# Performance work log

Measured on AMD Instinct MI355X. Metric: run time of the kernel, lower is better.

## Reference

```python
import jax, jax.numpy as jnp
import numpy as np

N_HARM_XYZ = 6
N_HARM_DIR = 4
HIDDEN_XYZ = 256
HIDDEN_DIR = 128
EMB_XYZ = N_HARM_XYZ * 2 * 3 + 3  # 39
EMB_DIR = N_HARM_DIR * 2 * 3 + 3  # 27


def harmonic_embedding(x, n_harmonics):
    # x: [..., 3] -> [..., n_harmonics*2*3 + 3]
    freqs = 2.0 ** jnp.arange(n_harmonics, dtype=x.dtype)  # logspace, omega0=1
    emb = (x[..., None] * freqs).reshape(*x.shape[:-1], -1)  # [..., 3*n_harm]
    return jnp.concatenate([jnp.sin(emb), jnp.cos(emb), x], axis=-1)


def setup_inputs() -> dict:
    key = jax.random.key(0)
    ks = jax.random.split(key, 32)
    R, P = 2048, 64
    inp = {
        'sample_points': jax.random.normal(ks[0], (R, P, 3), dtype=jnp.float32),
        'directions': jax.random.normal(ks[1], (R, 3), dtype=jnp.float32),
    }
    # trunk layer dims (skip concat before layer 5; last layer outputs hidden+1)
    dims_in = [EMB_XYZ, HIDDEN_XYZ, HIDDEN_XYZ, HIDDEN_XYZ, HIDDEN_XYZ,
               HIDDEN_XYZ + EMB_XYZ, HIDDEN_XYZ, HIDDEN_XYZ]
    dims_out = [HIDDEN_XYZ] * 7 + [HIDDEN_XYZ + 1]
    for i, (di, do) in enumerate(zip(dims_in, dims_out)):
        s = 1.0 / np.sqrt(di)
        inp[f'W{i}'] = jax.random.uniform(ks[2 + 2 * i], (di, do), jnp.float32, -s, s)
        inp[f'b{i}'] = jax.random.uniform(ks[3 + 2 * i], (do,), jnp.float32, -s, s)
    s = 1.0 / np.sqrt(HIDDEN_XYZ + EMB_DIR)
    inp['Wc'] = jax.random.uniform(ks[20], (HIDDEN_XYZ + EMB_DIR, HIDDEN_DIR), jnp.float32, -s, s)
    inp['bc'] = jax.random.uniform(ks[21], (HIDDEN_DIR,), jnp.float32, -s, s)
    s = 1.0 / np.sqrt(HIDDEN_DIR)
    inp['Wo'] = jax.random.uniform(ks[22], (HIDDEN_DIR, 3), jnp.float32, -s, s)
    inp['bo'] = jax.random.uniform(ks[23], (3,), jnp.float32, -s, s)
    return inp


def nerf_forward(sample_points, directions,
                 W0, b0, W1, b1, W2, b2, W3, b3, W4, b4, W5, b5, W6, b6, W7, b7,
                 Wc, bc, Wo, bo):
    R, P, _ = sample_points.shape
    pts = sample_points.reshape(-1, 3)              # [N, 3]
    e = harmonic_embedding(pts, N_HARM_XYZ)         # [N, 39]
    h = e
    # seq0: layers 0-4, ReLU after each
    for W, b in ((W0, b0), (W1, b1), (W2, b2), (W3, b3), (W4, b4)):
        h = jax.nn.relu(h @ W + b)
    # skip concat with xyz embedding, then seq1: layers 5-7 (no ReLU after last)
    h = jnp.concatenate([h, e], axis=-1)            # [N, 295]
    h = jax.nn.relu(h @ W5 + b5)
    h = jax.nn.relu(h @ W6 + b6)
    h = h @ W7 + b7                                  # [N, 257]
    sigma = jax.nn.relu(h[:, 0]).reshape(R, P, 1)
    dirs = jnp.broadcast_to(directions[:, None, :], (R, P, 3)).reshape(-1, 3)
    d = harmonic_embedding(dirs, N_HARM_DIR)         # [N, 27]
    c = jnp.concatenate([h[:, 1:], d], axis=-1)      # [N, 283]
    c = jax.nn.relu(c @ Wc + bc)
    color = jax.nn.sigmoid(c @ Wo + bo).reshape(R, P, 3)
    return color, sigma


def reference(sample_points, directions,
              W0, b0, W1, b1, W2, b2, W3, b3, W4, b4, W5, b5, W6, b6, W7, b7,
              Wc, bc, Wo, bo):
    # returns (feature, density) matching the torch dict values
    return nerf_forward(sample_points, directions,
                        W0, b0, W1, b1, W2, b2, W3, b3, W4, b4, W5, b5, W6, b6, W7, b7,
                        Wc, bc, Wo, bo)
```

## Files before the change

### kernel.cpp

```cpp
#include <hip/hip_runtime.h>

typedef __attribute__((ext_vector_type(8))) __bf16 bf16x8;
typedef __attribute__((ext_vector_type(4))) float float4_;
typedef __attribute__((ext_vector_type(4))) unsigned short ushort4_;
typedef __attribute__((ext_vector_type(8))) unsigned short ushort8_;

#define OFF_W0T 0
#define OFF_W1T 16384
#define OFF_W2T 81920
#define OFF_W3T 147456
#define OFF_W4T 212992
#define OFF_W5T 278528
#define OFF_W6T 360448
#define OFF_W7T 425984
#define OFF_WCT 491520
#define BF16_TOTAL 524288
#define WSF_BYTE_OFF (BF16_TOTAL * 2)

__device__ __forceinline__ unsigned short f2b(float v) {
  union { float f; unsigned u; } a; a.f = v;
  unsigned r = a.u + 0x7fffu + ((a.u >> 16) & 1u);
  return (unsigned short)(r >> 16);
}

__device__ __forceinline__ bf16x8 bzero() {
  union { ushort8_ u; bf16x8 b; } z;
  ushort8_ t = {0, 0, 0, 0, 0, 0, 0, 0};
  z.u = t;
  return z.b;
}

__device__ __forceinline__ ushort4_ pack4(float4_ v) {
#if __has_builtin(__builtin_amdgcn_cvt_pk_bf16_f32)
  auto p0 = __builtin_amdgcn_cvt_pk_bf16_f32(v.x, v.y);
  auto p1 = __builtin_amdgcn_cvt_pk_bf16_f32(v.z, v.w);
  union { decltype(p0) p; unsigned u; } u0, u1;
  u0.p = p0; u1.p = p1;
  ushort4_ r;
  r.x = (unsigned short)(u0.u & 0xffffu); r.y = (unsigned short)(u0.u >> 16);
  r.z = (unsigned short)(u1.u & 0xffffu); r.w = (unsigned short)(u1.u >> 16);
  return r;
#else
  ushort4_ r; r.x = f2b(v.x); r.y = f2b(v.y); r.z = f2b(v.z); r.w = f2b(v.w);
  return r;
#endif
}

__global__ __launch_bounds__(256) void prep_kernel(
    const float* __restrict__ W0, const float* __restrict__ W1,
    const float* __restrict__ W2, const float* __restrict__ W3,
    const float* __restrict__ W4, const float* __restrict__ W5,
    const float* __restrict__ W6, const float* __restrict__ W7,
    const float* __restrict__ Wc, const float* __restrict__ b7,
    unsigned short* __restrict__ wsb, float* __restrict__ wsf)
{
  int i = blockIdx.x * 256 + threadIdx.x;
  const float* src; int rs, K, n, k2, nt16; unsigned short* base;
  if (i < 8192)        { int t = i;          n = t & 255; k2 = t >> 8; src = W0; rs = 256; K = 39;  nt16 = 16; base = wsb + OFF_W0T; }
  else if (i < 139264) { int t = i - 8192;   int l = t >> 15; t &= 32767;
                         n = t & 255; k2 = t >> 8;
                         src = (l == 0) ? W1 : (l == 1) ? W2 : (l == 2) ? W3 : W4;
                         rs = 256; K = 256; nt16 = 16; base = wsb + OFF_W1T + l * 65536; }
  else if (i < 180224) { int t = i - 139264; n = t & 255; k2 = t >> 8; src = W5;     rs = 256; K = 295; nt16 = 16; base = wsb + OFF_W5T; }
  else if (i < 212992) { int t = i - 180224; n = t & 255; k2 = t >> 8; src = W6;     rs = 256; K = 256; nt16 = 16; base = wsb + OFF_W6T; }
  else if (i < 245760) { int t = i - 212992; n = t & 255; k2 = t >> 8; src = W7 + 1; rs = 257; K = 256; nt16 = 16; base = wsb + OFF_W7T; }
  else if (i < 262144) { int t = i - 245760; n = t & 127; k2 = t >> 7; src = Wc;     rs = 128; K = 256; nt16 = 8;  base = wsb + OFF_WCT; }
  else if (i < 262400) { int k = i - 262144; wsf[k] = W7[k * 257]; return; }
  else if (i < 262656) { int k = i - 262400; wsf[256 + k] = b7[k + 1]; return; }
  else return;
  const int k = k2 * 2;
  const float v0 = (k     < K) ? src[k * rs + n]       : 0.f;
  const float v1 = (k + 1 < K) ? src[(k + 1) * rs + n] : 0.f;
  const int off = ((k >> 5) * nt16 + (n >> 4)) * 512
                + ((k >> 3) & 3) * 128 + (n & 15) * 8 + (k & 7);
  const unsigned val = (unsigned)f2b(v0) | ((unsigned)f2b(v1) << 16);
  *(unsigned*)(base + off) = val;
}

template<int NT, int NTB, int KS1, int KS2, bool RELU>
__device__ __forceinline__ void layer_mm(
    const unsigned short* src1, const unsigned short* src2,
    const unsigned short* __restrict__ wT,
    const float* bias0, const float* bias1,
    unsigned short* dst, int lane, int wave)
{
  constexpr int KT = KS1 + KS2;
  const int c = lane & 15, q = lane >> 4;
  const int n0 = wave * (NT * 16);
  const unsigned short* wl = wT + (wave * NT) * 512 + lane * 8;

  float4_ acc[8][NT];
#pragma unroll
  for (int ni = 0; ni < NT; ++ni) {
    float4_ bv0 = *(const float4_*)(bias0 + n0 + ni * 16 + q * 4);
    float4_ bv1 = *(const float4_*)(bias1 + n0 + ni * 16 + q * 4);
#pragma unroll
    for (int mi = 0; mi < 8; ++mi) acc[mi][ni] = (mi < 4) ? bv0 : bv1;
  }

  bf16x8 aC[NT], aN[NT];
#pragma unroll
  for (int ni = 0; ni < NT; ++ni) aC[ni] = *(const bf16x8*)(wl + ni * 512);

#pragma unroll
  for (int ks = 0; ks < KT; ++ks) {
    if (ks + 1 < KT) {
#pragma unroll
      for (int ni = 0; ni < NT; ++ni)
        aN[ni] = *(const bf16x8*)(wl + ((ks + 1) * NTB + ni) * 512);
    }
#pragma unroll
    for (int mh = 0; mh < 4; ++mh) {
      bf16x8 bfr[2];
#pragma unroll
      for (int m2 = 0; m2 < 2; ++m2) {
        const int mi = mh * 2 + m2;
        if (ks < KS1) {
          bfr[m2] = *(const bf16x8*)(src1 + (ks * 8 + mi) * 512 + lane * 8);
        } else {
          const int kse = ks - KS1;
          bf16x8 ev = *(const bf16x8*)(src2 + (mi * 16 + c) * 40 + kse * 32 + q * 8);
          bfr[m2] = (kse == 0 || q == 0) ? ev : bzero();
        }
      }
#pragma unroll
      for (int ni = 0; ni < NT; ++ni)
#pragma unroll
        for (int m2 = 0; m2 < 2; ++m2)
          acc[mh * 2 + m2][ni] = __builtin_amdgcn_mfma_f32_16x16x32_bf16(
              aC[ni], bfr[m2], acc[mh * 2 + m2][ni], 0, 0, 0);
    }
    if (ks + 1 < KT) {
#pragma unroll
      for (int ni = 0; ni < NT; ++ni) aC[ni] = aN[ni];
    }
  }

  __syncthreads();
#pragma unroll
  for (int ni = 0; ni < NT; ++ni) {
    const int base = n0 + ni * 16 + q * 4;
#pragma unroll
    for (int mi = 0; mi < 8; ++mi) {
      float4_ v = acc[mi][ni];
      if (RELU) {
        v.x = fmaxf(v.x, 0.f); v.y = fmaxf(v.y, 0.f);
        v.z = fmaxf(v.z, 0.f); v.w = fmaxf(v.w, 0.f);
      }
      const int addr = ((base >> 5) * 8 + mi) * 512
                     + ((base >> 3) & 3) * 128 + c * 8 + (base & 7);
      *(ushort4_*)(dst + addr) = pack4(v);
    }
  }
  __syncthreads();
}

__global__ __launch_bounds__(512, 4) void nerf_kernel(
    const float* __restrict__ pts, const float* __restrict__ dirs,
    const float* __restrict__ b0, const float* __restrict__ b1,
    const float* __restrict__ b2, const float* __restrict__ b3,
    const float* __restrict__ b4, const float* __restrict__ b5,
    const float* __restrict__ b6, const float* __restrict__ b7,
    const float* __restrict__ Wc, const float* __restrict__ bc,
    const float* __restrict__ Wo, const float* __restrict__ bo,
    const unsigned short* __restrict__ wsb, const float* __restrict__ wsf,
    float* __restrict__ out)
{
  __shared__ __align__(16) unsigned short sAct[64 * 512];
  __shared__ __align__(16) unsigned short sEmb[128 * 40 + 64];
  __shared__ float s_dvec[54];
  __shared__ float s_biasc[256];

  const int blk = blockIdx.x;
  const int t = threadIdx.x;
  const int lane = t & 63;
  const int wave = t >> 6;

  {
    const int m = t >> 2, s4 = t & 3;
    const float* pb = pts + (blk * 128 + m) * 3;
    const float x0 = pb[0], x1 = pb[1], x2 = pb[2];
#pragma unroll
    for (int j = 0; j < 10; ++j) {
      const int cc = s4 * 10 + j;
      float v = 0.f;
      if (cc < 18) {
        const float xx = (cc < 6) ? x0 : (cc < 12) ? x1 : x2;
        v = sinf(xx * (float)(1 << (cc % 6)));
      } else if (cc < 36) {
        const int c2 = cc - 18;
        const float xx = (c2 < 6) ? x0 : (c2 < 12) ? x1 : x2;
        v = cosf(xx * (float)(1 << (c2 % 6)));
      } else if (cc == 36) v = x0;
      else if (cc == 37) v = x1;
      else if (cc == 38) v = x2;
      sEmb[m * 40 + cc] = f2b(v);
    }
  }
  if (t < 54) {
    const int r = (t >= 27) ? 1 : 0;
    const int j = t - r * 27;
    const float* db = dirs + (blk * 2 + r) * 3;
    float v;
    if (j < 12) v = sinf(db[j >> 2] * (float)(1 << (j & 3)));
    else if (j < 24) { const int j2 = j - 12; v = cosf(db[j2 >> 2] * (float)(1 << (j2 & 3))); }
    else v = db[j - 24];
    s_dvec[t] = v;
  }
  __syncthreads();
  if (t < 256) {
    const int r = t >> 7, n = t & 127;
    float s = bc[n];
#pragma unroll
    for (int j = 0; j < 27; ++j) s += s_dvec[r * 27 + j] * Wc[(256 + j) * 128 + n];
    s_biasc[t] = s;
  }

  layer_mm<2, 16, 0, 2, true >(sAct, sEmb, wsb + OFF_W0T, b0, b0, sAct, lane, wave);
  layer_mm<2, 16, 8, 0, true >(sAct, sEmb, wsb + OFF_W1T, b1, b1, sAct, lane, wave);
  layer_mm<2, 16, 8, 0, true >(sAct, sEmb, wsb + OFF_W2T, b2, b2, sAct, lane, wave);
  layer_mm<2, 16, 8, 0, true >(sAct, sEmb, wsb + OFF_W3T, b3, b3, sAct, lane, wave);
  layer_mm<2, 16, 8, 0, true >(sAct, sEmb, wsb + OFF_W4T, b4, b4, sAct, lane, wave);
  layer_mm<2, 16, 8, 2, true >(sAct, sEmb, wsb + OFF_W5T, b5, b5, sAct, lane, wave);
  layer_mm<2, 16, 8, 0, true >(sAct, sEmb, wsb + OFF_W6T, b6, b6, sAct, lane, wave);

  {
    const int m = t >> 2, q4 = t & 3;
    float s = 0.f;
#pragma unroll
    for (int i8 = 0; i8 < 8; ++i8) {
      const int kb = q4 * 64 + i8 * 8;
      bf16x8 hv = *(const bf16x8*)(sAct + ((kb >> 5) * 8 + (m >> 4)) * 512
                                       + ((kb >> 3) & 3) * 128 + (m & 15) * 8);
      const float* w = wsf + kb;
#pragma unroll
      for (int j = 0; j < 8; ++j) s += (float)hv[j] * w[j];
    }
    s += __shfl_xor(s, 1); s += __shfl_xor(s, 2);
    if (q4 == 0) out[393216 + blk * 128 + m] = fmaxf(s + b7[0], 0.f);
  }

  layer_mm<2, 16, 8, 0, false>(sAct, sEmb, wsb + OFF_W7T, wsf + 256, wsf + 256, sAct, lane, wave);
  layer_mm<1, 8,  8, 0, true >(sAct, sEmb, wsb + OFF_WCT, s_biasc, s_biasc + 128, sAct, lane, wave);

  {
    const int m = t >> 2, q4 = t & 3;
    float s0 = 0.f, s1 = 0.f, s2 = 0.f;
#pragma unroll
    for (int i8 = 0; i8 < 4; ++i8) {
      const int kb = q4 * 32 + i8 * 8;
      bf16x8 cv = *(const bf16x8*)(sAct + ((kb >> 5) * 8 + (m >> 4)) * 512
                                       + ((kb >> 3) & 3) * 128 + (m & 15) * 8);
#pragma unroll
      for (int j = 0; j < 8; ++j) {
        const float cc = (float)cv[j];
        const float* w = Wo + (kb + j) * 3;
        s0 += cc * w[0]; s1 += cc * w[1]; s2 += cc * w[2];
      }
    }
    s0 += __shfl_xor(s0, 1); s0 += __shfl_xor(s0, 2);
    s1 += __shfl_xor(s1, 1); s1 += __shfl_xor(s1, 2);
    s2 += __shfl_xor(s2, 1); s2 += __shfl_xor(s2, 2);
    if (q4 == 0) {
      float* oc = out + (blk * 128 + m) * 3;
      oc[0] = 1.f / (1.f + __expf(-(s0 + bo[0])));
      oc[1] = 1.f / (1.f + __expf(-(s1 + bo[1])));
      oc[2] = 1.f / (1.f + __expf(-(s2 + bo[2])));
    }
  }
}

extern "C" void kernel_launch(void* const* d_in, const int* in_sizes, int n_in,
                              void* d_out, int out_size, void* d_ws, size_t ws_size,
                              hipStream_t stream)
{
  const float* pts  = (const float*)d_in[0];
  const float* dirs = (const float*)d_in[1];
  const float* W0 = (const float*)d_in[2];   const float* b0 = (const float*)d_in[3];
  const float* W1 = (const float*)d_in[4];   const float* b1 = (const float*)d_in[5];
  const float* W2 = (const float*)d_in[6];   const float* b2 = (const float*)d_in[7];
  const float* W3 = (const float*)d_in[8];   const float* b3 = (const float*)d_in[9];
  const float* W4 = (const float*)d_in[10];  const float* b4 = (const float*)d_in[11];
  const float* W5 = (const float*)d_in[12];  const float* b5 = (const float*)d_in[13];
  const float* W6 = (const float*)d_in[14];  const float* b6 = (const float*)d_in[15];
  const float* W7 = (const float*)d_in[16];  const float* b7 = (const float*)d_in[17];
  const float* Wc = (const float*)d_in[18];  const float* bc = (const float*)d_in[19];
  const float* Wo = (const float*)d_in[20];  const float* bo = (const float*)d_in[21];

  unsigned short* wsb = (unsigned short*)d_ws;
  float* wsf = (float*)((char*)d_ws + WSF_BYTE_OFF);

  prep_kernel<<<1026, 256, 0, stream>>>(W0, W1, W2, W3, W4, W5, W6, W7, Wc, b7, wsb, wsf);
  nerf_kernel<<<1024, 512, 0, stream>>>(pts, dirs, b0, b1, b2, b3, b4, b5, b6, b7,
                                        Wc, bc, Wo, bo, wsb, wsf, (float*)d_out);
}
```

Baseline: 247.7 us.

## Halve per-block row tile to one ray and raise occupancy

```diff
diff --git a/kernel.cpp b/kernel.cpp
--- a/kernel.cpp
+++ b/kernel.cpp
@@ -81,7 +81,7 @@
 __device__ __forceinline__ void layer_mm(
     const unsigned short* src1, const unsigned short* src2,
     const unsigned short* __restrict__ wT,
-    const float* bias0, const float* bias1,
+    const float* bias,
     unsigned short* dst, int lane, int wave)
 {
   constexpr int KT = KS1 + KS2;
@@ -89,13 +89,12 @@
   const int n0 = wave * (NT * 16);
   const unsigned short* wl = wT + (wave * NT) * 512 + lane * 8;
 
-  float4_ acc[8][NT];
+  float4_ acc[4][NT];
 #pragma unroll
   for (int ni = 0; ni < NT; ++ni) {
-    float4_ bv0 = *(const float4_*)(bias0 + n0 + ni * 16 + q * 4);
-    float4_ bv1 = *(const float4_*)(bias1 + n0 + ni * 16 + q * 4);
-#pragma unroll
-    for (int mi = 0; mi < 8; ++mi) acc[mi][ni] = (mi < 4) ? bv0 : bv1;
+    float4_ bv = *(const float4_*)(bias + n0 + ni * 16 + q * 4);
+#pragma unroll
+    for (int m4 = 0; m4 < 4; ++m4) acc[m4][ni] = bv;
   }
 
   bf16x8 aC[NT], aN[NT];
@@ -110,13 +109,13 @@
         aN[ni] = *(const bf16x8*)(wl + ((ks + 1) * NTB + ni) * 512);
     }
 #pragma unroll
-    for (int mh = 0; mh < 4; ++mh) {
+    for (int mh = 0; mh < 2; ++mh) {
       bf16x8 bfr[2];
 #pragma unroll
       for (int m2 = 0; m2 < 2; ++m2) {
         const int mi = mh * 2 + m2;
         if (ks < KS1) {
-          bfr[m2] = *(const bf16x8*)(src1 + (ks * 8 + mi) * 512 + lane * 8);
+          bfr[m2] = *(const bf16x8*)(src1 + (ks * 4 + mi) * 512 + lane * 8);
         } else {
           const int kse = ks - KS1;
           bf16x8 ev = *(const bf16x8*)(src2 + (mi * 16 + c) * 40 + kse * 32 + q * 8);
@@ -141,13 +140,13 @@
   for (int ni = 0; ni < NT; ++ni) {
     const int base = n0 + ni * 16 + q * 4;
 #pragma unroll
-    for (int mi = 0; mi < 8; ++mi) {
-      float4_ v = acc[mi][ni];
+    for (int m4 = 0; m4 < 4; ++m4) {
+      float4_ v = acc[m4][ni];
       if (RELU) {
         v.x = fmaxf(v.x, 0.f); v.y = fmaxf(v.y, 0.f);
         v.z = fmaxf(v.z, 0.f); v.w = fmaxf(v.w, 0.f);
       }
-      const int addr = ((base >> 5) * 8 + mi) * 512
+      const int addr = ((base >> 5) * 4 + m4) * 512
                      + ((base >> 3) & 3) * 128 + c * 8 + (base & 7);
       *(ushort4_*)(dst + addr) = pack4(v);
     }
@@ -155,7 +154,7 @@
   __syncthreads();
 }
 
-__global__ __launch_bounds__(512, 4) void nerf_kernel(
+__global__ __launch_bounds__(512, 6) void nerf_kernel(
     const float* __restrict__ pts, const float* __restrict__ dirs,
     const float* __restrict__ b0, const float* __restrict__ b1,
     const float* __restrict__ b2, const float* __restrict__ b3,
@@ -166,23 +165,23 @@
     const unsigned short* __restrict__ wsb, const float* __restrict__ wsf,
     float* __restrict__ out)
 {
-  __shared__ __align__(16) unsigned short sAct[64 * 512];
-  __shared__ __align__(16) unsigned short sEmb[128 * 40 + 64];
-  __shared__ float s_dvec[54];
-  __shared__ float s_biasc[256];
-
-  const int blk = blockIdx.x;
+  __shared__ __align__(16) unsigned short sAct[32 * 512];
+  __shared__ __align__(16) unsigned short sEmb[64 * 40 + 32];
+  __shared__ float s_dvec[27];
+  __shared__ float s_biasc[128];
+
+  const int ray = blockIdx.x;
   const int t = threadIdx.x;
   const int lane = t & 63;
   const int wave = t >> 6;
 
   {
-    const int m = t >> 2, s4 = t & 3;
-    const float* pb = pts + (blk * 128 + m) * 3;
+    const int m = t >> 3, s8 = t & 7;
+    const float* pb = pts + (ray * 64 + m) * 3;
     const float x0 = pb[0], x1 = pb[1], x2 = pb[2];
 #pragma unroll
-    for (int j = 0; j < 10; ++j) {
-      const int cc = s4 * 10 + j;
+    for (int j = 0; j < 5; ++j) {
+      const int cc = s8 * 5 + j;
       float v = 0.f;
       if (cc < 18) {
         const float xx = (cc < 6) ? x0 : (cc < 12) ? x1 : x2;
@@ -197,59 +196,56 @@
       sEmb[m * 40 + cc] = f2b(v);
     }
   }
-  if (t < 54) {
-    const int r = (t >= 27) ? 1 : 0;
-    const int j = t - r * 27;
-    const float* db = dirs + (blk * 2 + r) * 3;
+  if (t < 27) {
+    const float* db = dirs + ray * 3;
     float v;
-    if (j < 12) v = sinf(db[j >> 2] * (float)(1 << (j & 3)));
-    else if (j < 24) { const int j2 = j - 12; v = cosf(db[j2 >> 2] * (float)(1 << (j2 & 3))); }
-    else v = db[j - 24];
+    if (t < 12) v = sinf(db[t >> 2] * (float)(1 << (t & 3)));
+    else if (t < 24) { const int j2 = t - 12; v = cosf(db[j2 >> 2] * (float)(1 << (j2 & 3))); }
+    else v = db[t - 24];
     s_dvec[t] = v;
   }
   __syncthreads();
-  if (t < 256) {
-    const int r = t >> 7, n = t & 127;
-    float s = bc[n];
-#pragma unroll
-    for (int j = 0; j < 27; ++j) s += s_dvec[r * 27 + j] * Wc[(256 + j) * 128 + n];
+  if (t < 128) {
+    float s = bc[t];
+#pragma unroll
+    for (int j = 0; j < 27; ++j) s += s_dvec[j] * Wc[(256 + j) * 128 + t];
     s_biasc[t] = s;
   }
 
-  layer_mm<2, 16, 0, 2, true >(sAct, sEmb, wsb + OFF_W0T, b0, b0, sAct, lane, wave);
-  layer_mm<2, 16, 8, 0, true >(sAct, sEmb, wsb + OFF_W1T, b1, b1, sAct, lane, wave);
-  layer_mm<2, 16, 8, 0, true >(sAct, sEmb, wsb + OFF_W2T, b2, b2, sAct, lane, wave);
-  layer_mm<2, 16, 8, 0, true >(sAct, sEmb, wsb + OFF_W3T, b3, b3, sAct, lane, wave);
-  layer_mm<2, 16, 8, 0, true >(sAct, sEmb, wsb + OFF_W4T, b4, b4, sAct, lane, wave);
-  layer_mm<2, 16, 8, 2, true >(sAct, sEmb, wsb + OFF_W5T, b5, b5, sAct, lane, wave);
-  layer_mm<2, 16, 8, 0, true >(sAct, sEmb, wsb + OFF_W6T, b6, b6, sAct, lane, wave);
+  layer_mm<2, 16, 0, 2, true >(sAct, sEmb, wsb + OFF_W0T, b0, sAct, lane, wave);
+  layer_mm<2, 16, 8, 0, true >(sAct, sEmb, wsb + OFF_W1T, b1, sAct, lane, wave);
+  layer_mm<2, 16, 8, 0, true >(sAct, sEmb, wsb + OFF_W2T, b2, sAct, lane, wave);
+  layer_mm<2, 16, 8, 0, true >(sAct, sEmb, wsb + OFF_W3T, b3, sAct, lane, wave);
+  layer_mm<2, 16, 8, 0, true >(sAct, sEmb, wsb + OFF_W4T, b4, sAct, lane, wave);
+  layer_mm<2, 16, 8, 2, true >(sAct, sEmb, wsb + OFF_W5T, b5, sAct, lane, wave);
+  layer_mm<2, 16, 8, 0, true >(sAct, sEmb, wsb + OFF_W6T, b6, sAct, lane, wave);
 
   {
-    const int m = t >> 2, q4 = t & 3;
+    const int m = t >> 3, q8 = t & 7;
     float s = 0.f;
 #pragma unroll
-    for (int i8 = 0; i8 < 8; ++i8) {
-      const int kb = q4 * 64 + i8 * 8;
-      bf16x8 hv = *(const bf16x8*)(sAct + ((kb >> 5) * 8 + (m >> 4)) * 512
+    for (int i8 = 0; i8 < 4; ++i8) {
+      const int kb = q8 * 32 + i8 * 8;
+      bf16x8 hv = *(const bf16x8*)(sAct + ((kb >> 5) * 4 + (m >> 4)) * 512
                                        + ((kb >> 3) & 3) * 128 + (m & 15) * 8);
       const float* w = wsf + kb;
 #pragma unroll
       for (int j = 0; j < 8; ++j) s += (float)hv[j] * w[j];
     }
-    s += __shfl_xor(s, 1); s += __shfl_xor(s, 2);
-    if (q4 == 0) out[393216 + blk * 128 + m] = fmaxf(s + b7[0], 0.f);
-  }
-
-  layer_mm<2, 16, 8, 0, false>(sAct, sEmb, wsb + OFF_W7T, wsf + 256, wsf + 256, sAct, lane, wave);
-  layer_mm<1, 8,  8, 0, true >(sAct, sEmb, wsb + OFF_WCT, s_biasc, s_biasc + 128, sAct, lane, wave);
+    s += __shfl_xor(s, 1); s += __shfl_xor(s, 2); s += __shfl_xor(s, 4);
+    if (q8 == 0) out[393216 + ray * 64 + m] = fmaxf(s + b7[0], 0.f);
+  }
+
+  layer_mm<2, 16, 8, 0, false>(sAct, sEmb, wsb + OFF_W7T, wsf + 256, sAct, lane, wave);
+  layer_mm<1, 8,  8, 0, true >(sAct, sEmb, wsb + OFF_WCT, s_biasc, sAct, lane, wave);
 
   {
-    const int m = t >> 2, q4 = t & 3;
+    const int m = t >> 3, q8 = t & 7;
     float s0 = 0.f, s1 = 0.f, s2 = 0.f;
 #pragma unroll
-    for (int i8 = 0; i8 < 4; ++i8) {
-      const int kb = q4 * 32 + i8 * 8;
-      bf16x8 cv = *(const bf16x8*)(sAct + ((kb >> 5) * 8 + (m >> 4)) * 512
+    for (int i2 = 0; i2 < 2; ++i2) {
+      const int kb = q8 * 16 + i2 * 8;
+      bf16x8 cv = *(const bf16x8*)(sAct + ((kb >> 5) * 4 + (m >> 4)) * 512
                                        + ((kb >> 3) & 3) * 128 + (m & 15) * 8);
 #pragma unroll
       for (int j = 0; j < 8; ++j) {
@@ -258,11 +254,11 @@
         s0 += cc * w[0]; s1 += cc * w[1]; s2 += cc * w[2];
       }
     }
-    s0 += __shfl_xor(s0, 1); s0 += __shfl_xor(s0, 2);
-    s1 += __shfl_xor(s1, 1); s1 += __shfl_xor(s1, 2);
-    s2 += __shfl_xor(s2, 1); s2 += __shfl_xor(s2, 2);
-    if (q4 == 0) {
-      float* oc = out + (blk * 128 + m) * 3;
+    s0 += __shfl_xor(s0, 1); s0 += __shfl_xor(s0, 2); s0 += __shfl_xor(s0, 4);
+    s1 += __shfl_xor(s1, 1); s1 += __shfl_xor(s1, 2); s1 += __shfl_xor(s1, 4);
+    s2 += __shfl_xor(s2, 1); s2 += __shfl_xor(s2, 2); s2 += __shfl_xor(s2, 4);
+    if (q8 == 0) {
+      float* oc = out + (ray * 64 + m) * 3;
       oc[0] = 1.f / (1.f + __expf(-(s0 + bo[0])));
       oc[1] = 1.f / (1.f + __expf(-(s1 + bo[1])));
       oc[2] = 1.f / (1.f + __expf(-(s2 + bo[2])));
@@ -291,6 +287,6 @@
   float* wsf = (float*)((char*)d_ws + WSF_BYTE_OFF);
 
   prep_kernel<<<1026, 256, 0, stream>>>(W0, W1, W2, W3, W4, W5, W6, W7, Wc, b7, wsb, wsf);
-  nerf_kernel<<<1024, 512, 0, stream>>>(pts, dirs, b0, b1, b2, b3, b4, b5, b6, b7,
+  nerf_kernel<<<2048, 512, 0, stream>>>(pts, dirs, b0, b1, b2, b3, b4, b5, b6, b7,
                                         Wc, bc, Wo, bo, wsb, wsf, (float*)d_out);
 }
```

Result: faster. 239.6 us, median of 2 (-3.3%).
